# Kernel optimization log

Measured on AMD Instinct MI355X. Metric: run time of the kernel, lower is better.

Reference implementation:

```python
import jax, jax.numpy as jnp
import numpy as np

H = 768      # hidden_size
NH = 12      # num_attention_heads
HD = H // NH # head_dim = 64
EPS = 1e-5


def setup_inputs() -> dict:
    key = jax.random.key(0)
    ks = jax.random.split(key, 12)
    B, S = 2, 2048
    s = 1.0 / np.sqrt(H)
    return {
        "hidden_states": jax.random.normal(ks[0], (B, S, H), dtype=jnp.float32),
        "attention_mask": jax.random.normal(ks[1], (B, S), dtype=jnp.float32),
        "Wq": jax.random.normal(ks[2], (H, H), dtype=jnp.float32) * s,
        "bq": jnp.zeros((H,), dtype=jnp.float32),
        "Wk": jax.random.normal(ks[3], (H, H), dtype=jnp.float32) * s,
        "bk": jnp.zeros((H,), dtype=jnp.float32),
        "Wv": jax.random.normal(ks[4], (H, H), dtype=jnp.float32) * s,
        "bv": jnp.zeros((H,), dtype=jnp.float32),
        "Wo": jax.random.normal(ks[5], (H, H), dtype=jnp.float32) * s,
        "bo": jnp.zeros((H,), dtype=jnp.float32),
        "ln_gamma": jnp.ones((H,), dtype=jnp.float32),
        "ln_beta": jnp.zeros((H,), dtype=jnp.float32),
    }


def reference(hidden_states, attention_mask, Wq, bq, Wk, bk, Wv, bv, Wo, bo, ln_gamma, ln_beta):
    B, S, E = hidden_states.shape
    # QKV projections -> [B, NH, S, HD]
    def proj(W, b):
        return (hidden_states @ W + b).reshape(B, S, NH, HD).transpose(0, 2, 1, 3)
    q = proj(Wq, bq)
    k = proj(Wk, bk)
    v = proj(Wv, bv)
    # scores [B, NH, S, S]
    att = jnp.einsum('bhqd,bhkd->bhqk', q, k) * (1.0 / np.sqrt(HD))
    # padding pair mask: valid iff mask>=0 at both query and key positions
    valid = (attention_mask >= 0)  # [B, S]
    pair = valid[:, None, :, None] & valid[:, None, None, :]  # [B,1,S,S]
    att = jnp.where(pair, att, -1e9)
    att = jax.nn.softmax(att, axis=-1)
    # dropout p=0 (eval) -> identity
    ctx = jnp.einsum('bhqk,bhkd->bhqd', att, v)  # [B,NH,S,HD]
    ctx = ctx.transpose(0, 2, 1, 3).reshape(B, S, E)
    # output dense + residual + LayerNorm
    h = ctx @ Wo + bo + hidden_states
    mu = jnp.mean(h, axis=-1, keepdims=True)
    var = jnp.mean(jnp.square(h - mu), axis=-1, keepdims=True)
    out = (h - mu) * jax.lax.rsqrt(var + EPS) * ln_gamma + ln_beta
    return out
```

## Files before the change

kernel.cpp:

```cpp
#include <hip/hip_runtime.h>
#include <hip/hip_bf16.h>

#define H_DIM 768
#define NHEAD 12
#define HDIM  64
#define S_LEN 2048
#define B_SZ  2
#define M_TOT (B_SZ * S_LEN)
#define NQKV  (3 * H_DIM)
#define LN_EPS 1e-5f
#define SM_C   0.1803368801f

typedef __attribute__((ext_vector_type(8)))  short bf16x8;
typedef __attribute__((ext_vector_type(4)))  float f32x4;
typedef __attribute__((ext_vector_type(16))) float f32x16;
typedef __attribute__((ext_vector_type(4)))  int   i32x4;

static __device__ inline ushort f2bf(float x) {
    __hip_bfloat16 h = __float2bfloat16(x);
    ushort u;
    __builtin_memcpy(&u, &h, 2);
    return u;
}
static __device__ inline float bf2f(ushort u) {
    unsigned int v = ((unsigned int)u) << 16;
    float f;
    __builtin_memcpy(&f, &v, 4);
    return f;
}
static __device__ inline unsigned cvt_pk_bf16(float lo, float hi) {
    unsigned r;
    asm("v_cvt_pk_bf16_f32 %0, %1, %2" : "=v"(r) : "v"(lo), "v"(hi));
    return r;
}

#define GLDS16(g, l) __builtin_amdgcn_global_load_lds( \
    (const __attribute__((address_space(1))) void*)(g), \
    (__attribute__((address_space(3))) void*)(l), 16, 0, 0)

__global__ __launch_bounds__(256)
void prep(const float* __restrict__ hs,
          const float* __restrict__ Wq, const float* __restrict__ Wk,
          const float* __restrict__ Wv, const float* __restrict__ Wo,
          const float* __restrict__ bq, const float* __restrict__ bk,
          const float* __restrict__ bv,
          ushort* __restrict__ Xbf, ushort* __restrict__ Wcat,
          ushort* __restrict__ Wot, float* __restrict__ bcat)
{
    __shared__ ushort T[64][65];
    const int bid = blockIdx.x;
    const int t   = threadIdx.x;

    if (bid < 3072) {
        const int i = (bid * 256 + t) * 4;
        f32x4 v = *(const f32x4*)(hs + i);
        ushort4 o;
        o.x = f2bf(v[0]); o.y = f2bf(v[1]); o.z = f2bf(v[2]); o.w = f2bf(v[3]);
        *(ushort4*)(Xbf + i) = o;
    } else if (bid < 3072 + 576) {
        const int bid2 = bid - 3072;
        const int z = bid2 / 144;
        const int rem = bid2 % 144;
        const int n0 = (rem / 12) * 64;
        const int k0 = (rem % 12) * 64;
        const float* W = (z == 0) ? Wq : (z == 1) ? Wk : (z == 2) ? Wv : Wo;
        const int r = t >> 2, c0 = (t & 3) * 16;
        const float* src = W + (size_t)(k0 + r) * H_DIM + n0 + c0;
        #pragma unroll
        for (int j = 0; j < 16; j += 4) {
            f32x4 v = *(const f32x4*)(src + j);
            #pragma unroll
            for (int jj = 0; jj < 4; ++jj) T[r][c0 + j + jj] = f2bf(v[jj]);
        }
        __syncthreads();
        bf16x8 o0, o1;
        #pragma unroll
        for (int j = 0; j < 8; ++j) {
            o0[j] = (short)T[c0 + j][r];
            o1[j] = (short)T[c0 + 8 + j][r];
        }
        ushort* dst = (z < 3)
            ? Wcat + (size_t)(z * 768 + n0 + r) * H_DIM + k0 + c0
            : Wot  + (size_t)(n0 + r) * H_DIM + k0 + c0;
        *(bf16x8*)dst       = o0;
        *(bf16x8*)(dst + 8) = o1;
    } else {
        const int i = (bid - 3648) * 256 + t;
        if (i < NQKV) {
            float v = (i < 768) ? bq[i] : (i < 1536) ? bk[i - 768] : bv[i - 1536];
            bcat[i] = v;
        }
    }
}

__global__ __launch_bounds__(256)
void gemm_mfma(const ushort* __restrict__ A, const ushort* __restrict__ Bt,
               const float* __restrict__ bias, void* __restrict__ outp,
               ushort* __restrict__ vtp, int M, int N, int K,
               int nscale, float sfac)
{
    __shared__ ushort As[128 * 32];
    __shared__ ushort Bs[128 * 32];
    const int bn = blockIdx.x * 128;
    const int bm = blockIdx.y * 128;
    const int t  = threadIdx.x;
    const int w  = t >> 6, l = t & 63;
    const int lg = l >> 4, lr = l & 15;
    const int wr = w >> 1, wc = w & 1;

    f32x4 acc[4][4];
    #pragma unroll
    for (int i = 0; i < 4; ++i)
        #pragma unroll
        for (int j = 0; j < 4; ++j) acc[i][j] = (f32x4){0.f, 0.f, 0.f, 0.f};

    for (int k0 = 0; k0 < K; k0 += 32) {
        #pragma unroll
        for (int it = 0; it < 2; ++it) {
            const int g = it * 256 + t;
            const int r = g >> 2, cb = (g & 3) * 8;
            GLDS16(A  + (size_t)(bm + r) * K + k0 + cb, (char*)As + g * 16);
            GLDS16(Bt + (size_t)(bn + r) * K + k0 + cb, (char*)Bs + g * 16);
        }
        __syncthreads();
        bf16x8 af[4], bfr[4];
        #pragma unroll
        for (int m16 = 0; m16 < 4; ++m16)
            af[m16] = *(const bf16x8*)&As[(wr * 64 + m16 * 16 + lr) * 32 + lg * 8];
        #pragma unroll
        for (int n16 = 0; n16 < 4; ++n16)
            bfr[n16] = *(const bf16x8*)&Bs[(wc * 64 + n16 * 16 + lr) * 32 + lg * 8];
        #pragma unroll
        for (int m16 = 0; m16 < 4; ++m16)
            #pragma unroll
            for (int n16 = 0; n16 < 4; ++n16)
                acc[m16][n16] = __builtin_amdgcn_mfma_f32_16x16x32_bf16(
                    af[m16], bfr[n16], acc[m16][n16], 0, 0, 0);
        __syncthreads();
    }

    #pragma unroll
    for (int m16 = 0; m16 < 4; ++m16) {
        #pragma unroll
        for (int n16 = 0; n16 < 4; ++n16) {
            const int col = bn + wc * 64 + n16 * 16 + lr;
            const float bcol = bias[col];
            const int row0 = bm + wr * 64 + m16 * 16 + lg * 4;
            float vv[4];
            #pragma unroll
            for (int r = 0; r < 4; ++r) {
                float v = acc[m16][n16][r] + bcol;
                if (col < nscale) v *= sfac;
                vv[r] = v;
            }
            if (col >= 1536) {
                const int dfull = col - 1536;
                const int hh = dfull >> 6, dd = dfull & 63;
                const int bb = row0 >> 11, ss = row0 & 2047;
                ushort4 pk;
                pk.x = f2bf(vv[0]); pk.y = f2bf(vv[1]);
                pk.z = f2bf(vv[2]); pk.w = f2bf(vv[3]);
                *(ushort4*)(vtp + ((size_t)(bb * NHEAD + hh) * HDIM + dd) * S_LEN + ss) = pk;
            } else {
                #pragma unroll
                for (int r = 0; r < 4; ++r)
                    ((ushort*)outp)[(size_t)(row0 + r) * N + col] = f2bf(vv[r]);
            }
        }
    }
}

__global__ __launch_bounds__(256)
void gemm_out96(const ushort* __restrict__ A, const ushort* __restrict__ Bt,
                const float* __restrict__ bias, const float* __restrict__ resid,
                ushort* __restrict__ outp)
{
    __shared__ ushort As[64 * 32];
    __shared__ ushort Bs[96 * 32];
    const int bn = blockIdx.x * 96;
    const int bm = blockIdx.y * 64;
    const int t  = threadIdx.x;
    const int w  = t >> 6, l = t & 63;
    const int lg = l >> 4, lr = l & 15;
    const int wr = w >> 1, wc = w & 1;

    f32x4 acc[2][3];
    #pragma unroll
    for (int i = 0; i < 2; ++i)
        #pragma unroll
        for (int j = 0; j < 3; ++j) acc[i][j] = (f32x4){0.f, 0.f, 0.f, 0.f};

    for (int k0 = 0; k0 < H_DIM; k0 += 32) {
        {
            const int r = t >> 2, cb = (t & 3) * 8;
            GLDS16(A + (size_t)(bm + r) * H_DIM + k0 + cb, (char*)As + t * 16);
        }
        {
            const int r = t >> 2, cb = (t & 3) * 8;
            GLDS16(Bt + (size_t)(bn + r) * H_DIM + k0 + cb, (char*)Bs + t * 16);
            if (t < 128) {
                const int g = 256 + t;
                const int r2 = g >> 2, cb2 = (g & 3) * 8;
                GLDS16(Bt + (size_t)(bn + r2) * H_DIM + k0 + cb2, (char*)Bs + g * 16);
            }
        }
        __syncthreads();
        bf16x8 af[2], bfr[3];
        #pragma unroll
        for (int m16 = 0; m16 < 2; ++m16)
            af[m16] = *(const bf16x8*)&As[(wr * 32 + m16 * 16 + lr) * 32 + lg * 8];
        #pragma unroll
        for (int n16 = 0; n16 < 3; ++n16)
            bfr[n16] = *(const bf16x8*)&Bs[(wc * 48 + n16 * 16 + lr) * 32 + lg * 8];
        #pragma unroll
        for (int m16 = 0; m16 < 2; ++m16)
            #pragma unroll
            for (int n16 = 0; n16 < 3; ++n16)
                acc[m16][n16] = __builtin_amdgcn_mfma_f32_16x16x32_bf16(
                    af[m16], bfr[n16], acc[m16][n16], 0, 0, 0);
        __syncthreads();
    }

    #pragma unroll
    for (int m16 = 0; m16 < 2; ++m16) {
        #pragma unroll
        for (int n16 = 0; n16 < 3; ++n16) {
            const int col = bn + wc * 48 + n16 * 16 + lr;
            const float bcol = bias[col];
            const int row0 = bm + wr * 32 + m16 * 16 + lg * 4;
            #pragma unroll
            for (int r = 0; r < 4; ++r) {
                float v = acc[m16][n16][r] + bcol
                        + resid[(size_t)(row0 + r) * H_DIM + col];
                outp[(size_t)(row0 + r) * H_DIM + col] = f2bf(v);
            }
        }
    }
}

#define KT     64
#define ATT_QT 128
#define KVHALF (S_LEN / 2)
#define NTILES (KVHALF / KT)

__global__ __launch_bounds__(256, 3)
void attn_mfma(const ushort* __restrict__ Qbf, const ushort* __restrict__ Kbf,
               const ushort* __restrict__ Vt, const float* __restrict__ mask,
               ushort* __restrict__ Pp, float* __restrict__ lp)
{
    const int flat = blockIdx.x;
    const int wk   = (flat & 7) * 96 + (flat >> 3);
    const int qt   = wk & 15;
    const int c_   = wk >> 4;
    const int h    = c_ % 12;
    const int bz   = c_ / 12;
    const int b    = bz >> 1, half = bz & 1;

    const int t  = threadIdx.x;
    const int w  = t >> 6, l = t & 63;
    const int l31 = l & 31, hi = l >> 5;
    const int q0 = qt * ATT_QT;
    const int kb0 = half * KVHALF;

    __shared__ ushort Ks[3][KT][64];
    __shared__ ushort Vs[2][HDIM][64];
    __shared__ float  kmarg[KVHALF];

    {
        const int i = t * 4;
        f32x4 v = *(const f32x4*)(mask + b * S_LEN + kb0 + i);
        f32x4 o;
        #pragma unroll
        for (int j = 0; j < 4; ++j)
            o[j] = (v[j] >= 0.f) ? 0.f : -1e30f;
        *(f32x4*)&kmarg[i] = o;
    }

    const bool qnL = (mask[b * S_LEN + q0 + w * 32 + l31] < 0.f);

    bf16x8 qa[4];
    {
        const ushort* qsrc = Qbf + (size_t)(b * S_LEN + q0 + w * 32 + l31) * NQKV
                           + h * HDIM + 8 * hi;
        #pragma unroll
        for (int k = 0; k < 4; ++k)
            qa[k] = *(const bf16x8*)(qsrc + 16 * k);
    }

    const int u    = l >> 3;
    const int scol = ((l & 7) ^ u) * 8;
    const int srcK = w * 16 + u + ((u & 4) ? 4 : 0);
    const int srow = w * 16 + u;
    const ushort* kLane = Kbf + (size_t)(b * S_LEN + kb0 + srcK) * NQKV
                        + h * HDIM + scol;
    const ushort* vLane = Vt + ((size_t)(b * NHEAD + h) * HDIM + srow) * S_LEN
                        + kb0 + scol;
    char* ldsK = (char*)Ks + w * 2048 + l * 16;
    char* ldsV = (char*)Vs + w * 2048 + l * 16;

    __syncthreads();

    GLDS16(kLane, ldsK);
    GLDS16(kLane + (size_t)4 * NQKV, ldsK + 1024);
    GLDS16(vLane, ldsV);
    GLDS16(vLane + (size_t)8 * S_LEN, ldsV + 1024);
    GLDS16(kLane + (size_t)KT * NQKV, ldsK + 8192);
    GLDS16(kLane + (size_t)(KT + 4) * NQKV, ldsK + 8192 + 1024);

    float l_part = 0.f;
    f32x16 accO[2];
    #pragma unroll
    for (int dt = 0; dt < 2; ++dt)
        #pragma unroll
        for (int i = 0; i < 16; ++i) accO[dt][i] = 0.f;

    const int swzl = (l31 & 7) << 4;

    for (int tt = 0; tt < NTILES; ++tt) {
        if (tt < NTILES - 1) {
            asm volatile("s_waitcnt vmcnt(2)" ::: "memory");
        } else {
            asm volatile("s_waitcnt vmcnt(0)" ::: "memory");
        }
        __builtin_amdgcn_s_barrier();

        if (tt + 1 < NTILES) {
            const ushort* vsrc = vLane + (size_t)(tt + 1) * KT;
            char* lv = ldsV + ((tt + 1) & 1) * 8192;
            GLDS16(vsrc, lv);
            GLDS16(vsrc + (size_t)8 * S_LEN, lv + 1024);
            if (tt + 2 < NTILES) {
                const ushort* ksrc = kLane + (size_t)(tt + 2) * KT * NQKV;
                char* lk = ldsK + ((tt + 2) % 3) * 8192;
                GLDS16(ksrc, lk);
                GLDS16(ksrc + (size_t)4 * NQKV, lk + 1024);
            }
        }

        const char* Kc = (const char*)Ks + (tt % 3) * 8192;
        const char* Vc = (const char*)Vs + (tt & 1) * 8192;

        #pragma unroll
        for (int kvt = 0; kvt < 2; ++kvt) {
            f32x16 sc;
            __builtin_amdgcn_s_setprio(1);
            {
                const char* abase = Kc + (kvt * 32 + l31) * 128;
                bf16x8 a0 = *(const bf16x8*)(abase + ((16 * hi +  0) ^ swzl));
                bf16x8 a1 = *(const bf16x8*)(abase + ((16 * hi + 32) ^ swzl));
                bf16x8 a2 = *(const bf16x8*)(abase + ((16 * hi + 64) ^ swzl));
                bf16x8 a3 = *(const bf16x8*)(abase + ((16 * hi + 96) ^ swzl));
                f32x16 z;
                #pragma unroll
                for (int i = 0; i < 16; ++i) z[i] = 0.f;
                sc = __builtin_amdgcn_mfma_f32_32x32x16_bf16(a0, qa[0], z, 0, 0, 0);
                sc = __builtin_amdgcn_mfma_f32_32x32x16_bf16(a1, qa[1], sc, 0, 0, 0);
                sc = __builtin_amdgcn_mfma_f32_32x32x16_bf16(a2, qa[2], sc, 0, 0, 0);
                sc = __builtin_amdgcn_mfma_f32_32x32x16_bf16(a3, qa[3], sc, 0, 0, 0);
            }
            __builtin_amdgcn_s_setprio(0);

            float p[16];
            const float* km = &kmarg[tt * 64 + kvt * 32];
            #pragma unroll
            for (int q4 = 0; q4 < 4; ++q4) {
                const int kvb = 16 * (q4 >> 1) + 8 * hi + 4 * (q4 & 1);
                f32x4 kq = *(const f32x4*)(km + kvb);
                #pragma unroll
                for (int r = 0; r < 4; ++r) {
                    float arg = sc[q4 * 4 + r] + kq[r];
                    arg = qnL ? 0.f : arg;
                    const float pv = exp2f(arg);
                    p[q4 * 4 + r] = pv;
                    l_part += pv;
                }
            }

            __builtin_amdgcn_s_setprio(1);
            #pragma unroll
            for (int cc = 0; cc < 2; ++cc) {
                i32x4 pku;
                pku[0] = (int)cvt_pk_bf16(p[8 * cc + 0], p[8 * cc + 1]);
                pku[1] = (int)cvt_pk_bf16(p[8 * cc + 2], p[8 * cc + 3]);
                pku[2] = (int)cvt_pk_bf16(p[8 * cc + 4], p[8 * cc + 5]);
                pku[3] = (int)cvt_pk_bf16(p[8 * cc + 6], p[8 * cc + 7]);
                bf16x8 pa;
                __builtin_memcpy(&pa, &pku, 16);
                const int c = kvt * 2 + cc;
                #pragma unroll
                for (int dt = 0; dt < 2; ++dt) {
                    bf16x8 bv = *(const bf16x8*)(Vc + (32 * dt + l31) * 128
                                                 + ((32 * c + 16 * hi) ^ swzl));
                    accO[dt] = __builtin_amdgcn_mfma_f32_32x32x16_bf16(
                        pa, bv, accO[dt], 0, 0, 0);
                }
            }
            __builtin_amdgcn_s_setprio(0);
        }
    }

    l_part += __shfl_xor(l_part, 32, 64);

    const size_t MN = (size_t)M_TOT * H_DIM;
    #pragma unroll
    for (int dt = 0; dt < 2; ++dt) {
        #pragma unroll
        for (int reg = 0; reg < 16; ++reg) {
            const int q = (reg & 3) + 8 * (reg >> 2) + 4 * hi;
            const int m = b * S_LEN + q0 + w * 32 + q;
            Pp[(size_t)half * MN + (size_t)m * H_DIM + h * HDIM + 32 * dt + l31]
                = f2bf(accO[dt][reg]);
        }
    }
    if (hi == 0) {
        const int m = b * S_LEN + q0 + w * 32 + l31;
        lp[half * (M_TOT * NHEAD) + m * NHEAD + h] = l_part;
    }
}

__global__ __launch_bounds__(256)
void combine_kernel(const ushort* __restrict__ Pp, const float* __restrict__ lp,
                    ushort* __restrict__ ctx)
{
    const int idx = blockIdx.x * 256 + threadIdx.x;
    const int m  = idx / 96;
    const int c8 = idx % 96;
    const int c  = c8 * 8;
    const int h  = c8 >> 3;
    const size_t MN = (size_t)M_TOT * H_DIM;

    const float lsum = lp[m * NHEAD + h] + lp[M_TOT * NHEAD + m * NHEAD + h];
    const float inv  = 1.0f / lsum;

    bf16x8 a = *(const bf16x8*)(Pp + (size_t)m * H_DIM + c);
    bf16x8 b = *(const bf16x8*)(Pp + MN + (size_t)m * H_DIM + c);
    bf16x8 o;
    #pragma unroll
    for (int j = 0; j < 8; ++j)
        o[j] = (short)f2bf((bf2f((ushort)a[j]) + bf2f((ushort)b[j])) * inv);
    *(bf16x8*)(ctx + (size_t)m * H_DIM + c) = o;
}

__global__ __launch_bounds__(256)
void ln_kernel(const ushort* __restrict__ Hbuf, const float* __restrict__ gamma,
               const float* __restrict__ beta, float* __restrict__ out)
{
    const int m = blockIdx.x * 4 + (threadIdx.x >> 6);
    const int l = threadIdx.x & 63;
    const ushort* row = Hbuf + (size_t)m * H_DIM;

    float x[12];
    #pragma unroll
    for (int k = 0; k < 3; ++k) {
        ushort4 v = *(const ushort4*)(row + l * 4 + k * 256);
        x[k * 4 + 0] = bf2f(v.x);
        x[k * 4 + 1] = bf2f(v.y);
        x[k * 4 + 2] = bf2f(v.z);
        x[k * 4 + 3] = bf2f(v.w);
    }

    float s = 0.f;
    #pragma unroll
    for (int j = 0; j < 12; ++j) s += x[j];
    #pragma unroll
    for (int off = 1; off < 64; off <<= 1) s += __shfl_xor(s, off, 64);
    const float mu = s * (1.0f / H_DIM);

    float v = 0.f;
    #pragma unroll
    for (int j = 0; j < 12; ++j) {
        const float d = x[j] - mu;
        v += d * d;
    }
    #pragma unroll
    for (int off = 1; off < 64; off <<= 1) v += __shfl_xor(v, off, 64);
    const float rstd = rsqrtf(v * (1.0f / H_DIM) + LN_EPS);

    #pragma unroll
    for (int k = 0; k < 3; ++k) {
        const int c = l * 4 + k * 256;
        f32x4 gm = *(const f32x4*)(gamma + c);
        f32x4 bt = *(const f32x4*)(beta + c);
        f32x4 o;
        #pragma unroll
        for (int j = 0; j < 4; ++j)
            o[j] = (x[k * 4 + j] - mu) * rstd * gm[j] + bt[j];
        *(f32x4*)(out + (size_t)m * H_DIM + c) = o;
    }
}

extern "C" void kernel_launch(void* const* d_in, const int* in_sizes, int n_in,
                              void* d_out, int out_size, void* d_ws, size_t ws_size,
                              hipStream_t stream)
{
    const float* hs   = (const float*)d_in[0];
    const float* mask = (const float*)d_in[1];
    const float* Wq   = (const float*)d_in[2];
    const float* bq   = (const float*)d_in[3];
    const float* Wk   = (const float*)d_in[4];
    const float* bk   = (const float*)d_in[5];
    const float* Wv   = (const float*)d_in[6];
    const float* bv   = (const float*)d_in[7];
    const float* Wo   = (const float*)d_in[8];
    const float* bo   = (const float*)d_in[9];
    const float* g    = (const float*)d_in[10];
    const float* be   = (const float*)d_in[11];
    float* out = (float*)d_out;

    char* base = (char*)d_ws;
    ushort* Xbf    = (ushort*)(base);
    ushort* QKVbf  = (ushort*)(base + 6291456);
    ushort* Wcat   = (ushort*)(base + 25165824);
    ushort* Wot    = (ushort*)(base + 28704768);
    float*  bcat   = (float*) (base + 29884416);
    ushort* Vt     = (ushort*)(base + 29893632);
    ushort* Cbf    = (ushort*)(base + 36185088);
    ushort* Pp     = (ushort*)(base + 42476544);
    float*  lp     = (float*) (base + 25165824);
    ushort* Hb2    = Xbf;

    prep<<<3657, 256, 0, stream>>>(hs, Wq, Wk, Wv, Wo, bq, bk, bv,
                                   Xbf, Wcat, Wot, bcat);

    gemm_mfma<<<dim3(NQKV / 128, M_TOT / 128), 256, 0, stream>>>(
        Xbf, Wcat, bcat, QKVbf, Vt, M_TOT, NQKV, H_DIM, 768, SM_C);

    attn_mfma<<<768, 256, 0, stream>>>(
        QKVbf, QKVbf + 768, Vt, mask, Pp, lp);

    combine_kernel<<<M_TOT * 96 / 256, 256, 0, stream>>>(Pp, lp, Cbf);

    gemm_out96<<<dim3(H_DIM / 96, M_TOT / 64), 256, 0, stream>>>(
        Cbf, Wot, bo, hs, Hb2);

    ln_kernel<<<M_TOT / 4, 256, 0, stream>>>(Hb2, g, be, out);
}
```

Measured before the change: 116.6 us.

## Fuse split-KV combine into output GEMM and retile QKV GEMM to 128x96

Removes the separate combine kernel: the output projection GEMM now loads both partial attention outputs and row sums, normalizes and converts to bf16 while filling its A tile in shared memory. This drops one launch and the write and re-read of the intermediate context buffer, but the combine work is now repeated by every column block of the output GEMM, and the A tile uses plain register loads and stores instead of direct global-to-LDS loads. Separately, the QKV GEMM tile changes from 128x128 to 128x96, giving 768 blocks with a remapped block order that groups blocks across XCDs, for better CU occupancy and cache locality.

```diff
diff --git a/kernel.cpp b/kernel.cpp
--- a/kernel.cpp
+++ b/kernel.cpp
@@ -94,46 +94,55 @@
 }
 
 __global__ __launch_bounds__(256)
-void gemm_mfma(const ushort* __restrict__ A, const ushort* __restrict__ Bt,
-               const float* __restrict__ bias, void* __restrict__ outp,
-               ushort* __restrict__ vtp, int M, int N, int K,
-               int nscale, float sfac)
+void gemm_qkv(const ushort* __restrict__ A, const ushort* __restrict__ Bt,
+              const float* __restrict__ bias, ushort* __restrict__ outp,
+              ushort* __restrict__ vtp)
 {
     __shared__ ushort As[128 * 32];
-    __shared__ ushort Bs[128 * 32];
-    const int bn = blockIdx.x * 128;
-    const int bm = blockIdx.y * 128;
+    __shared__ ushort Bs[96 * 32];
+    const int flat = blockIdx.x;
+    const int wkb  = (flat & 7) * 96 + (flat >> 3);
+    const int bn   = (wkb % 24) * 96;
+    const int bm   = (wkb / 24) * 128;
     const int t  = threadIdx.x;
     const int w  = t >> 6, l = t & 63;
     const int lg = l >> 4, lr = l & 15;
     const int wr = w >> 1, wc = w & 1;
 
-    f32x4 acc[4][4];
+    f32x4 acc[4][3];
     #pragma unroll
     for (int i = 0; i < 4; ++i)
         #pragma unroll
-        for (int j = 0; j < 4; ++j) acc[i][j] = (f32x4){0.f, 0.f, 0.f, 0.f};
-
-    for (int k0 = 0; k0 < K; k0 += 32) {
+        for (int j = 0; j < 3; ++j) acc[i][j] = (f32x4){0.f, 0.f, 0.f, 0.f};
+
+    for (int k0 = 0; k0 < H_DIM; k0 += 32) {
         #pragma unroll
         for (int it = 0; it < 2; ++it) {
             const int g = it * 256 + t;
             const int r = g >> 2, cb = (g & 3) * 8;
-            GLDS16(A  + (size_t)(bm + r) * K + k0 + cb, (char*)As + g * 16);
-            GLDS16(Bt + (size_t)(bn + r) * K + k0 + cb, (char*)Bs + g * 16);
+            GLDS16(A + (size_t)(bm + r) * H_DIM + k0 + cb, (char*)As + g * 16);
+        }
+        {
+            const int r = t >> 2, cb = (t & 3) * 8;
+            GLDS16(Bt + (size_t)(bn + r) * H_DIM + k0 + cb, (char*)Bs + t * 16);
+            if (t < 128) {
+                const int g = 256 + t;
+                const int r2 = g >> 2, cb2 = (g & 3) * 8;
+                GLDS16(Bt + (size_t)(bn + r2) * H_DIM + k0 + cb2, (char*)Bs + g * 16);
+            }
         }
         __syncthreads();
-        bf16x8 af[4], bfr[4];
+        bf16x8 af[4], bfr[3];
         #pragma unroll
         for (int m16 = 0; m16 < 4; ++m16)
             af[m16] = *(const bf16x8*)&As[(wr * 64 + m16 * 16 + lr) * 32 + lg * 8];
         #pragma unroll
-        for (int n16 = 0; n16 < 4; ++n16)
-            bfr[n16] = *(const bf16x8*)&Bs[(wc * 64 + n16 * 16 + lr) * 32 + lg * 8];
+        for (int n16 = 0; n16 < 3; ++n16)
+            bfr[n16] = *(const bf16x8*)&Bs[(wc * 48 + n16 * 16 + lr) * 32 + lg * 8];
         #pragma unroll
         for (int m16 = 0; m16 < 4; ++m16)
             #pragma unroll
-            for (int n16 = 0; n16 < 4; ++n16)
+            for (int n16 = 0; n16 < 3; ++n16)
                 acc[m16][n16] = __builtin_amdgcn_mfma_f32_16x16x32_bf16(
                     af[m16], bfr[n16], acc[m16][n16], 0, 0, 0);
         __syncthreads();
@@ -142,15 +151,15 @@
     #pragma unroll
     for (int m16 = 0; m16 < 4; ++m16) {
         #pragma unroll
-        for (int n16 = 0; n16 < 4; ++n16) {
-            const int col = bn + wc * 64 + n16 * 16 + lr;
+        for (int n16 = 0; n16 < 3; ++n16) {
+            const int col = bn + wc * 48 + n16 * 16 + lr;
             const float bcol = bias[col];
             const int row0 = bm + wr * 64 + m16 * 16 + lg * 4;
             float vv[4];
             #pragma unroll
             for (int r = 0; r < 4; ++r) {
                 float v = acc[m16][n16][r] + bcol;
-                if (col < nscale) v *= sfac;
+                if (col < 768) v *= SM_C;
                 vv[r] = v;
             }
             if (col >= 1536) {
@@ -164,16 +173,16 @@
             } else {
                 #pragma unroll
                 for (int r = 0; r < 4; ++r)
-                    ((ushort*)outp)[(size_t)(row0 + r) * N + col] = f2bf(vv[r]);
+                    outp[(size_t)(row0 + r) * NQKV + col] = f2bf(vv[r]);
             }
         }
     }
 }
 
 __global__ __launch_bounds__(256)
-void gemm_out96(const ushort* __restrict__ A, const ushort* __restrict__ Bt,
-                const float* __restrict__ bias, const float* __restrict__ resid,
-                ushort* __restrict__ outp)
+void gemm_out96(const ushort* __restrict__ Pp, const float* __restrict__ lp,
+                const ushort* __restrict__ Bt, const float* __restrict__ bias,
+                const float* __restrict__ resid, ushort* __restrict__ outp)
 {
     __shared__ ushort As[64 * 32];
     __shared__ ushort Bs[96 * 32];
@@ -183,6 +192,7 @@
     const int w  = t >> 6, l = t & 63;
     const int lg = l >> 4, lr = l & 15;
     const int wr = w >> 1, wc = w & 1;
+    const size_t MN = (size_t)M_TOT * H_DIM;
 
     f32x4 acc[2][3];
     #pragma unroll
@@ -193,7 +203,23 @@
     for (int k0 = 0; k0 < H_DIM; k0 += 32) {
         {
             const int r = t >> 2, cb = (t & 3) * 8;
-            GLDS16(A + (size_t)(bm + r) * H_DIM + k0 + cb, (char*)As + t * 16);
+            const int m = bm + r;
+            const int c = k0 + cb;
+            const int hh = k0 >> 6;
+            bf16x8 a0 = *(const bf16x8*)(Pp + (size_t)m * H_DIM + c);
+            bf16x8 a1 = *(const bf16x8*)(Pp + MN + (size_t)m * H_DIM + c);
+            const float inv = 1.0f /
+                (lp[m * NHEAD + hh] + lp[M_TOT * NHEAD + m * NHEAD + hh]);
+            bf16x8 o;
+            #pragma unroll
+            for (int j = 0; j < 8; j += 2) {
+                float x0 = (bf2f((ushort)a0[j])     + bf2f((ushort)a1[j]))     * inv;
+                float x1 = (bf2f((ushort)a0[j + 1]) + bf2f((ushort)a1[j + 1])) * inv;
+                unsigned pk = cvt_pk_bf16(x0, x1);
+                o[j]     = (short)(pk & 0xffff);
+                o[j + 1] = (short)(pk >> 16);
+            }
+            *(bf16x8*)&As[t * 8] = o;
         }
         {
             const int r = t >> 2, cb = (t & 3) * 8;
@@ -416,29 +442,6 @@
         const int m = b * S_LEN + q0 + w * 32 + l31;
         lp[half * (M_TOT * NHEAD) + m * NHEAD + h] = l_part;
     }
-}
-
-__global__ __launch_bounds__(256)
-void combine_kernel(const ushort* __restrict__ Pp, const float* __restrict__ lp,
-                    ushort* __restrict__ ctx)
-{
-    const int idx = blockIdx.x * 256 + threadIdx.x;
-    const int m  = idx / 96;
-    const int c8 = idx % 96;
-    const int c  = c8 * 8;
-    const int h  = c8 >> 3;
-    const size_t MN = (size_t)M_TOT * H_DIM;
-
-    const float lsum = lp[m * NHEAD + h] + lp[M_TOT * NHEAD + m * NHEAD + h];
-    const float inv  = 1.0f / lsum;
-
-    bf16x8 a = *(const bf16x8*)(Pp + (size_t)m * H_DIM + c);
-    bf16x8 b = *(const bf16x8*)(Pp + MN + (size_t)m * H_DIM + c);
-    bf16x8 o;
-    #pragma unroll
-    for (int j = 0; j < 8; ++j)
-        o[j] = (short)f2bf((bf2f((ushort)a[j]) + bf2f((ushort)b[j])) * inv);
-    *(bf16x8*)(ctx + (size_t)m * H_DIM + c) = o;
 }
 
 __global__ __launch_bounds__(256)
@@ -514,7 +517,6 @@
     ushort* Wot    = (ushort*)(base + 28704768);
     float*  bcat   = (float*) (base + 29884416);
     ushort* Vt     = (ushort*)(base + 29893632);
-    ushort* Cbf    = (ushort*)(base + 36185088);
     ushort* Pp     = (ushort*)(base + 42476544);
     float*  lp     = (float*) (base + 25165824);
     ushort* Hb2    = Xbf;
@@ -522,16 +524,13 @@
     prep<<<3657, 256, 0, stream>>>(hs, Wq, Wk, Wv, Wo, bq, bk, bv,
                                    Xbf, Wcat, Wot, bcat);
 
-    gemm_mfma<<<dim3(NQKV / 128, M_TOT / 128), 256, 0, stream>>>(
-        Xbf, Wcat, bcat, QKVbf, Vt, M_TOT, NQKV, H_DIM, 768, SM_C);
+    gemm_qkv<<<768, 256, 0, stream>>>(Xbf, Wcat, bcat, QKVbf, Vt);
 
     attn_mfma<<<768, 256, 0, stream>>>(
         QKVbf, QKVbf + 768, Vt, mask, Pp, lp);
 
-    combine_kernel<<<M_TOT * 96 / 256, 256, 0, stream>>>(Pp, lp, Cbf);
-
     gemm_out96<<<dim3(H_DIM / 96, M_TOT / 64), 256, 0, stream>>>(
-        Cbf, Wot, bo, hs, Hb2);
+        Pp, lp, Wot, bo, hs, Hb2);
 
     ln_kernel<<<M_TOT / 4, 256, 0, stream>>>(Hb2, g, be, out);
 }
```

After: 120.2 us. +3.1%, slower.
